# Kernel optimization log

Measured on AMD Instinct MI355X. Metric: run time of the kernel, lower is better.

Reference implementation:

```python
import jax, jax.numpy as jnp
import numpy as np

D_MODEL = 1024
N_HEADS = 16
HEAD_DIM = D_MODEL // N_HEADS
BATCH = 4
SEQ = 2048


def setup_inputs() -> dict:
    key = jax.random.key(0)
    ks = jax.random.split(key, 5)
    # Xavier uniform bound for square d_model x d_model weights
    bound = np.sqrt(6.0 / (D_MODEL + D_MODEL))
    x = jax.random.normal(ks[0], (BATCH, SEQ, D_MODEL), dtype=jnp.float32)
    attention_mask = jnp.ones((BATCH, SEQ), dtype=jnp.int32)
    wq = jax.random.uniform(ks[1], (D_MODEL, D_MODEL), jnp.float32, -bound, bound)
    wk = jax.random.uniform(ks[2], (D_MODEL, D_MODEL), jnp.float32, -bound, bound)
    wv = jax.random.uniform(ks[3], (D_MODEL, D_MODEL), jnp.float32, -bound, bound)
    wo = jax.random.uniform(ks[4], (D_MODEL, D_MODEL), jnp.float32, -bound, bound)
    return {"x": x, "attention_mask": attention_mask,
            "wq": wq, "wk": wk, "wv": wv, "wo": wo}


def reference(x, attention_mask, wq, wk, wv, wo):
    # x: (B, S, D). Linear weights stored torch-style (out, in): y = x @ W^T
    B, S, D = x.shape
    H, Hd = N_HEADS, HEAD_DIM
    scale = np.sqrt(Hd).astype(np.float32)

    def split_heads(t):  # (B,S,D) -> (B,H,S,Hd)
        return t.reshape(B, S, H, Hd).transpose(0, 2, 1, 3)

    q = split_heads(jnp.einsum('bsd,ed->bse', x, wq))
    k = split_heads(jnp.einsum('bsd,ed->bse', x, wk))
    v = split_heads(jnp.einsum('bsd,ed->bse', x, wv))

    scores = jnp.einsum('bhqd,bhkd->bhqk', q, k) / scale  # (B,H,S,S)

    causal = jnp.tril(jnp.ones((S, S), dtype=bool))  # True = keep
    keep = causal[None, None, :, :] & (attention_mask[:, None, None, :] != 0)
    scores = jnp.where(keep, scores, -jnp.inf)

    attn = jax.nn.softmax(scores, axis=-1)  # dropout: eval mode (identity)
    out = jnp.einsum('bhqk,bhkd->bhqd', attn, v)  # (B,H,S,Hd)
    out = out.transpose(0, 2, 1, 3).reshape(B, S, D)
    return jnp.einsum('bsd,ed->bse', out, wo)
```

## Files before the change

kernel.cpp:

```cpp
#include <hip/hip_runtime.h>
#include <cstdint>
#include <cstddef>

#define D_MODEL 1024
#define N_HEADS 16
#define HEAD_DIM 64
#define BATCH 4
#define SEQ 2048
#define M_TOTAL (BATCH * SEQ)

typedef __attribute__((ext_vector_type(8))) short bf16x8;
typedef __attribute__((ext_vector_type(4))) float f32x4;
typedef __attribute__((ext_vector_type(16))) float f32x16;

#define Q_SCALE 0.18033688011112042f

__device__ __forceinline__ unsigned short f2bu(float f) {
    union { float f; unsigned u; } x; x.f = f;
    unsigned r = x.u + 0x7FFFu + ((x.u >> 16) & 1u);
    return (unsigned short)(r >> 16);
}

__device__ __forceinline__ void async16(void* lds, const void* g) {
    __builtin_amdgcn_global_load_lds(
        (const __attribute__((address_space(1))) void*)g,
        (__attribute__((address_space(3))) void*)lds, 16, 0, 0);
}

__global__ __launch_bounds__(256) void cast_all(const float* __restrict__ x,
                                                const float* __restrict__ wq,
                                                const float* __restrict__ wk,
                                                const float* __restrict__ wv,
                                                const float* __restrict__ wo,
                                                unsigned short* __restrict__ dst) {
    const size_t NE = (size_t)M_TOTAL * D_MODEL;
    const size_t WE = (size_t)D_MODEL * D_MODEL;
    size_t i4 = (size_t)blockIdx.x * 256 + threadIdx.x;
    size_t e = i4 * 4;
    const float* src; size_t off;
    if (e < NE) { src = x; off = e; }
    else {
        size_t t = e - NE;
        int r = (int)(t / WE); off = t - (size_t)r * WE;
        src = (r == 0) ? wq : (r == 1) ? wk : (r == 2) ? wv : wo;
    }
    float4 v = *(const float4*)(src + off);
    ushort4 o;
    o.x = f2bu(v.x); o.y = f2bu(v.y); o.z = f2bu(v.z); o.w = f2bu(v.w);
    ((ushort4*)dst)[i4] = o;
}

__global__ __launch_bounds__(256) void qkv_gemm(const unsigned short* __restrict__ X,
                                                const unsigned short* __restrict__ W0,
                                                const unsigned short* __restrict__ W1,
                                                const unsigned short* __restrict__ W2,
                                                unsigned short* __restrict__ Y0,
                                                unsigned short* __restrict__ Y1,
                                                unsigned short* __restrict__ Vt) {
    __shared__ short As[128 * 32];
    __shared__ short Bs[128 * 32];

    const int id = (int)blockIdx.x + 24 * (int)blockIdx.y;
    const int xcd = id & 7, slot = id >> 3;
    const int ty = xcd * 8 + slot / 24;
    const int tx = slot % 24;

    const int sel = tx >> 3;
    const unsigned short* W = (sel == 0) ? W0 : (sel == 1) ? W1 : W2;
    const float scl = (sel == 0) ? Q_SCALE : 1.0f;

    const int tid = threadIdx.x;
    const int w = tid >> 6, lane = tid & 63, quad = lane >> 4, l15 = lane & 15;
    const int wm = w & 1, wn = w >> 1;
    const int rowBase = ty * 128;
    const int colBase = (tx & 7) * 128;

    f32x4 acc[4][4];
#pragma unroll
    for (int mi = 0; mi < 4; ++mi)
#pragma unroll
        for (int ni = 0; ni < 4; ++ni)
#pragma unroll
            for (int e = 0; e < 4; ++e) acc[mi][ni][e] = 0.f;

    for (int k0 = 0; k0 < 1024; k0 += 32) {
        __syncthreads();
#pragma unroll
        for (int l = 0; l < 2; ++l) {
            int c = tid + l * 256;
            int row = c >> 2, ccs = c & 3;
            int cc = ccs ^ ((row >> 1) & 3);
            async16((char*)As + c * 16, X + (size_t)(rowBase + row) * 1024 + k0 + cc * 8);
            async16((char*)Bs + c * 16, W + (size_t)(colBase + row) * 1024 + k0 + cc * 8);
        }
        __syncthreads();

        bf16x8 a[4], b[4];
#pragma unroll
        for (int mi = 0; mi < 4; ++mi) {
            int r = wm * 64 + mi * 16 + l15;
            int slt = quad ^ ((r >> 1) & 3);
            a[mi] = *(const bf16x8*)&As[r * 32 + slt * 8];
        }
#pragma unroll
        for (int ni = 0; ni < 4; ++ni) {
            int r = wn * 64 + ni * 16 + l15;
            int slt = quad ^ ((r >> 1) & 3);
            b[ni] = *(const bf16x8*)&Bs[r * 32 + slt * 8];
        }
#pragma unroll
        for (int mi = 0; mi < 4; ++mi)
#pragma unroll
            for (int ni = 0; ni < 4; ++ni)
                acc[mi][ni] = __builtin_amdgcn_mfma_f32_16x16x32_bf16(a[mi], b[ni], acc[mi][ni], 0, 0, 0);
    }

    if (sel != 2) {
        unsigned short* Y = (sel == 0) ? Y0 : Y1;
#pragma unroll
        for (int mi = 0; mi < 4; ++mi)
#pragma unroll
            for (int ni = 0; ni < 4; ++ni)
#pragma unroll
                for (int reg = 0; reg < 4; ++reg) {
                    int row = rowBase + wm * 64 + mi * 16 + quad * 4 + reg;
                    int col = colBase + wn * 64 + ni * 16 + l15;
                    Y[(size_t)row * 1024 + col] = f2bu(acc[mi][ni][reg] * scl);
                }
    } else {
#pragma unroll
        for (int mi = 0; mi < 4; ++mi) {
            int row0 = rowBase + wm * 64 + mi * 16 + quad * 4;
            int bb = row0 >> 11;
            int s0 = row0 & 2047;
#pragma unroll
            for (int ni = 0; ni < 4; ++ni) {
                int col = colBase + wn * 64 + ni * 16 + l15;
                int hh = col >> 6, dd = col & 63;
                ushort4 pk;
                pk.x = f2bu(acc[mi][ni][0]); pk.y = f2bu(acc[mi][ni][1]);
                pk.z = f2bu(acc[mi][ni][2]); pk.w = f2bu(acc[mi][ni][3]);
                *(ushort4*)(Vt + (((size_t)bb * 16 + hh) * 64 + dd) * SEQ + s0) = pk;
            }
        }
    }
}

__global__ __launch_bounds__(256) void out_gemm(const unsigned short* __restrict__ X,
                                                const unsigned short* __restrict__ W,
                                                float* __restrict__ Y) {
    __shared__ short As[128 * 32];
    __shared__ short Bs[128 * 32];

    const int id = (int)blockIdx.x + 8 * (int)blockIdx.y;
    const int xcd = id & 7, slot = id >> 3;
    const int ty = xcd * 8 + (slot >> 3);
    const int tx = slot & 7;

    const int tid = threadIdx.x;
    const int w = tid >> 6, lane = tid & 63, quad = lane >> 4, l15 = lane & 15;
    const int wm = w & 1, wn = w >> 1;
    const int rowBase = ty * 128;
    const int colBase = tx * 128;

    f32x4 acc[4][4];
#pragma unroll
    for (int mi = 0; mi < 4; ++mi)
#pragma unroll
        for (int ni = 0; ni < 4; ++ni)
#pragma unroll
            for (int e = 0; e < 4; ++e) acc[mi][ni][e] = 0.f;

    for (int k0 = 0; k0 < 1024; k0 += 32) {
        __syncthreads();
#pragma unroll
        for (int l = 0; l < 2; ++l) {
            int c = tid + l * 256;
            int row = c >> 2, ccs = c & 3;
            int cc = ccs ^ ((row >> 1) & 3);
            async16((char*)As + c * 16, X + (size_t)(rowBase + row) * 1024 + k0 + cc * 8);
            async16((char*)Bs + c * 16, W + (size_t)(colBase + row) * 1024 + k0 + cc * 8);
        }
        __syncthreads();

        bf16x8 a[4], b[4];
#pragma unroll
        for (int mi = 0; mi < 4; ++mi) {
            int r = wm * 64 + mi * 16 + l15;
            int slt = quad ^ ((r >> 1) & 3);
            a[mi] = *(const bf16x8*)&As[r * 32 + slt * 8];
        }
#pragma unroll
        for (int ni = 0; ni < 4; ++ni) {
            int r = wn * 64 + ni * 16 + l15;
            int slt = quad ^ ((r >> 1) & 3);
            b[ni] = *(const bf16x8*)&Bs[r * 32 + slt * 8];
        }
#pragma unroll
        for (int mi = 0; mi < 4; ++mi)
#pragma unroll
            for (int ni = 0; ni < 4; ++ni)
                acc[mi][ni] = __builtin_amdgcn_mfma_f32_16x16x32_bf16(a[mi], b[ni], acc[mi][ni], 0, 0, 0);
    }

#pragma unroll
    for (int mi = 0; mi < 4; ++mi)
#pragma unroll
        for (int ni = 0; ni < 4; ++ni)
#pragma unroll
            for (int reg = 0; reg < 4; ++reg) {
                int row = rowBase + wm * 64 + mi * 16 + quad * 4 + reg;
                int col = colBase + wn * 64 + ni * 16 + l15;
                Y[(size_t)row * 1024 + col] = acc[mi][ni][reg];
            }
}

__global__ __launch_bounds__(256) void flash32(const unsigned short* __restrict__ Q,
                                               const unsigned short* __restrict__ K,
                                               const unsigned short* __restrict__ Vt,
                                               const int* __restrict__ mask,
                                               unsigned short* __restrict__ CTX) {
    __shared__ short lds[16384];
    __shared__ float biasS[2][64];
    __shared__ int allokS[2];
    __shared__ int okW[4];

    const int bh = blockIdx.x;
    const int pid = blockIdx.y;
    const int b = bh >> 4;
    const int tid = threadIdx.x;
    const int w = tid >> 6, lane = tid & 63, l31 = lane & 31, lane5 = lane >> 5;

    const size_t qkBase = (size_t)b * SEQ * D_MODEL + (size_t)(bh & 15) * HEAD_DIM;
    const size_t vtBase = (size_t)bh * HEAD_DIM * SEQ;

    {
        int ok = 1;
        for (int i = tid; i < SEQ; i += 256) ok &= (mask[b * SEQ + i] != 0);
        unsigned long long bal = __ballot(ok != 0);
        if (lane == 0) okW[w] = (bal == ~0ull) ? 1 : 0;
    }
    __syncthreads();
    const int allSeq = okW[0] & okW[1] & okW[2] & okW[3];

    int stp[2], stcc[2], stj[2];
#pragma unroll
    for (int l = 0; l < 2; ++l) {
        int c = tid + l * 256;
        int p = c >> 3, sl = c & 7;
        stp[l] = p;
        stcc[l] = sl ^ (p & 7);
        stj[l] = (p & 0x33) | ((p & 4) << 1) | ((p & 8) >> 1);
    }

    for (int phase = 0; phase < 2; ++phase) {
        const int qt = phase ? pid : 15 - pid;
        const int q0 = qt * 128;
        const int iq = q0 + w * 32 + l31;

        bf16x8 qf[4];
#pragma unroll
        for (int ks = 0; ks < 4; ++ks)
            qf[ks] = *(const bf16x8*)(Q + qkBase + (size_t)iq * D_MODEL + ks * 16 + lane5 * 8);

        float mv = -INFINITY, lv = 0.f;
        f32x16 Ot[2];
#pragma unroll
        for (int dt = 0; dt < 2; ++dt)
#pragma unroll
            for (int e = 0; e < 16; ++e) Ot[dt][e] = 0.f;

        const int ktmax = 2 * qt + 1;

        uint4 kreg[2], vreg[2];
        int mreg = 1;
#pragma unroll
        for (int l = 0; l < 2; ++l) {
            kreg[l] = *(const uint4*)(K + qkBase + (size_t)stj[l] * D_MODEL + stcc[l] * 8);
            vreg[l] = *(const uint4*)(Vt + vtBase + (size_t)stp[l] * SEQ + stcc[l] * 8);
        }
        if (!allSeq && tid < 64) mreg = mask[b * SEQ + tid];

        for (int kt = 0; kt <= ktmax; ++kt) {
            const int k0 = kt * 64;
            const int buf = kt & 1;
#pragma unroll
            for (int l = 0; l < 2; ++l) {
                int c = tid + l * 256;
                *(uint4*)((char*)lds + buf * 8192 + c * 16) = kreg[l];
                *(uint4*)((char*)lds + 16384 + buf * 8192 + c * 16) = vreg[l];
            }
            if (!allSeq && tid < 64) {
                biasS[buf][tid] = mreg ? 0.f : -INFINITY;
                unsigned long long bal = __ballot(mreg != 0);
                if (tid == 0) allokS[buf] = (bal == ~0ull) ? 1 : 0;
            }
            if (kt < ktmax) {
                const int kn = k0 + 64;
#pragma unroll
                for (int l = 0; l < 2; ++l) {
                    kreg[l] = *(const uint4*)(K + qkBase + (size_t)(kn + stj[l]) * D_MODEL + stcc[l] * 8);
                    vreg[l] = *(const uint4*)(Vt + vtBase + (size_t)stp[l] * SEQ + kn + stcc[l] * 8);
                }
                if (!allSeq && tid < 64) mreg = mask[b * SEQ + kn + tid];
            }
            __syncthreads();

            if (64 * kt > q0 + 32 * w + 31) continue;

            const short* Ks = lds + buf * 4096;
            const short* Vs = lds + 8192 + buf * 4096;

            const int kHi = q0 + 32 * w + 31 - k0;
            const int nT = (kHi >= 32) ? 2 : 1;
            const int nt = ((kHi >> 4) >= 3 ? 3 : (kHi >> 4)) + 1;

            f32x16 St[2];
            __builtin_amdgcn_s_setprio(1);
#pragma unroll
            for (int T = 0; T < 2; ++T) {
                if (T < nT) {
#pragma unroll
                    for (int e = 0; e < 16; ++e) St[T][e] = 0.f;
#pragma unroll
                    for (int ks = 0; ks < 4; ++ks) {
                        int p = T * 32 + l31;
                        int slot = (ks * 2 + lane5) ^ (p & 7);
                        bf16x8 a = *(const bf16x8*)&Ks[p * 64 + slot * 8];
                        St[T] = __builtin_amdgcn_mfma_f32_32x32x16_bf16(a, qf[ks], St[T], 0, 0, 0);
                    }
                }
            }
            __builtin_amdgcn_s_setprio(0);

            const bool partial = (k0 + 63 > q0 + 32 * w);
            if (partial) {
#pragma unroll
                for (int T = 0; T < 2; ++T)
                    if (T < nT)
#pragma unroll
                        for (int r = 0; r < 16; ++r) {
                            int j = k0 + 32 * T + 16 * (r >> 3) + 8 * lane5 + (r & 7);
                            if (j > iq) St[T][r] = -INFINITY;
                        }
            }
            if (!allSeq && !allokS[buf]) {
#pragma unroll
                for (int T = 0; T < 2; ++T)
                    if (T < nT)
#pragma unroll
                        for (int r = 0; r < 16; ++r)
                            St[T][r] += biasS[buf][32 * T + 16 * (r >> 3) + 8 * lane5 + (r & 7)];
            }

            float tm[2];
#pragma unroll
            for (int T = 0; T < 2; ++T) {
                if (T < nT) {
                    float a0 = fmaxf(fmaxf(St[T][0], St[T][1]), fmaxf(St[T][2], St[T][3]));
                    float a1 = fmaxf(fmaxf(St[T][4], St[T][5]), fmaxf(St[T][6], St[T][7]));
                    float a2 = fmaxf(fmaxf(St[T][8], St[T][9]), fmaxf(St[T][10], St[T][11]));
                    float a3 = fmaxf(fmaxf(St[T][12], St[T][13]), fmaxf(St[T][14], St[T][15]));
                    tm[T] = fmaxf(fmaxf(a0, a1), fmaxf(a2, a3));
                } else tm[T] = -INFINITY;
            }
            float rm = fmaxf(tm[0], tm[1]);
            rm = fmaxf(rm, __shfl_xor(rm, 32));
            float mn = fmaxf(mv, rm);
            if (mn > mv + 8.f) {
                float al = exp2f(mv - mn);
                lv *= al;
#pragma unroll
                for (int dt = 0; dt < 2; ++dt)
#pragma unroll
                    for (int e = 0; e < 16; ++e) Ot[dt][e] *= al;
                mv = mn;
            }
            float rsp[2] = {0.f, 0.f};
#pragma unroll
            for (int T = 0; T < 2; ++T) {
                if (T < nT) {
#pragma unroll
                    for (int r = 0; r < 16; ++r) {
                        float pv = exp2f(St[T][r] - mv);
                        St[T][r] = pv;
                        rsp[T] += pv;
                    }
                }
            }
            float rs = rsp[0] + rsp[1];
            rs += __shfl_xor(rs, 32);
            lv += rs;

            bf16x8 pf[4];
#pragma unroll
            for (int t = 0; t < 4; ++t) {
                if (t < nt) {
                    const int T = t >> 1, hb = t & 1;
                    unsigned u0, u1, u2, u3;
                    asm("v_cvt_pk_bf16_f32 %0, %1, %2" : "=v"(u0)
                        : "v"(St[T][hb * 8 + 0]), "v"(St[T][hb * 8 + 1]));
                    asm("v_cvt_pk_bf16_f32 %0, %1, %2" : "=v"(u1)
                        : "v"(St[T][hb * 8 + 2]), "v"(St[T][hb * 8 + 3]));
                    asm("v_cvt_pk_bf16_f32 %0, %1, %2" : "=v"(u2)
                        : "v"(St[T][hb * 8 + 4]), "v"(St[T][hb * 8 + 5]));
                    asm("v_cvt_pk_bf16_f32 %0, %1, %2" : "=v"(u3)
                        : "v"(St[T][hb * 8 + 6]), "v"(St[T][hb * 8 + 7]));
                    union { unsigned u[4]; bf16x8 v; } pk;
                    pk.u[0] = u0; pk.u[1] = u1; pk.u[2] = u2; pk.u[3] = u3;
                    pf[t] = pk.v;
                }
            }

            __builtin_amdgcn_s_setprio(1);
#pragma unroll
            for (int dt = 0; dt < 2; ++dt)
#pragma unroll
                for (int t = 0; t < 4; ++t) {
                    if (t < nt) {
                        int p = dt * 32 + l31;
                        int slot = (t * 2 + lane5) ^ (p & 7);
                        bf16x8 a = *(const bf16x8*)&Vs[p * 64 + slot * 8];
                        Ot[dt] = __builtin_amdgcn_mfma_f32_32x32x16_bf16(a, pf[t], Ot[dt], 0, 0, 0);
                    }
                }
            __builtin_amdgcn_s_setprio(0);
        }

        __syncthreads();
        const float inv = 1.f / lv;
#pragma unroll
        for (int dt = 0; dt < 2; ++dt)
#pragma unroll
            for (int k = 0; k < 8; ++k) {
                int r0 = 2 * k;
                int d = (r0 & 3) + 4 * lane5 + 8 * (r0 >> 2) + 32 * dt;
                unsigned lo = f2bu(Ot[dt][r0] * inv);
                unsigned hi = f2bu(Ot[dt][r0 + 1] * inv);
                *(unsigned*)&lds[(w * 32 + l31) * 72 + d] = lo | (hi << 16);
            }
        __syncthreads();
#pragma unroll
        for (int k = 0; k < 4; ++k) {
            int id = tid + k * 256;
            int r = id >> 3, cc = id & 7;
            uint4 v = *(const uint4*)&lds[r * 72 + cc * 8];
            *(uint4*)(CTX + qkBase + (size_t)(q0 + r) * D_MODEL + cc * 8) = v;
        }
        __syncthreads();
    }
}

extern "C" void kernel_launch(void* const* d_in, const int* in_sizes, int n_in,
                              void* d_out, int out_size, void* d_ws, size_t ws_size,
                              hipStream_t stream) {
    const float* x  = (const float*)d_in[0];
    const int* mask = (const int*)d_in[1];
    const float* wq = (const float*)d_in[2];
    const float* wk = (const float*)d_in[3];
    const float* wv = (const float*)d_in[4];
    const float* wo = (const float*)d_in[5];
    float* out = (float*)d_out;

    const size_t NE = (size_t)M_TOTAL * D_MODEL;
    const size_t WE = (size_t)D_MODEL * D_MODEL;
    unsigned short* ws  = (unsigned short*)d_ws;
    unsigned short* xb  = ws;
    unsigned short* wqb = xb + NE;
    unsigned short* wkb = wqb + WE;
    unsigned short* wvb = wkb + WE;
    unsigned short* wob = wvb + WE;
    unsigned short* Qb  = wob + WE;
    unsigned short* Kb  = Qb + NE;
    unsigned short* Vtb = Kb + NE;
    unsigned short* CTX = Vtb + NE;

    cast_all<<<(int)((NE + 4 * WE) / 4 / 256), 256, 0, stream>>>(x, wq, wk, wv, wo, ws);

    qkv_gemm<<<dim3(24, M_TOTAL / 128), 256, 0, stream>>>(xb, wqb, wkb, wvb, Qb, Kb, Vtb);

    flash32<<<dim3(64, 8), 256, 0, stream>>>(Qb, Kb, Vtb, mask, CTX);

    out_gemm<<<dim3(D_MODEL / 128, M_TOTAL / 128), 256, 0, stream>>>(CTX, wob, out);
}
```

Baseline: 306.7 us.

## Split flash attention KV range in two halves and merge with a combine kernel

The causal KV range of each query tile is split into two halves, doubling the attention grid so more blocks are resident per CU; the launch bound also requests higher occupancy. Each half writes unnormalized bf16 partial outputs plus per-row max and sum into scratch, reusing the x and wq cast buffers that are dead after the QKV GEMM. A new elementwise kernel rescales and merges the two partials into the context buffer. The merge adds an extra read/write pass over the context plus a launch, and storing unnormalized partials in bf16 adds a rounding step.

```diff
diff --git a/kernel.cpp b/kernel.cpp
--- a/kernel.cpp
+++ b/kernel.cpp
@@ -19,6 +19,9 @@
     union { float f; unsigned u; } x; x.f = f;
     unsigned r = x.u + 0x7FFFu + ((x.u >> 16) & 1u);
     return (unsigned short)(r >> 16);
+}
+__device__ __forceinline__ float bu2f(unsigned hi16bits) {
+    union { unsigned u; float f; } x; x.u = hi16bits; return x.f;
 }
 
 __device__ __forceinline__ void async16(void* lds, const void* g) {
@@ -215,18 +218,21 @@
             }
 }
 
-__global__ __launch_bounds__(256) void flash32(const unsigned short* __restrict__ Q,
-                                               const unsigned short* __restrict__ K,
-                                               const unsigned short* __restrict__ Vt,
-                                               const int* __restrict__ mask,
-                                               unsigned short* __restrict__ CTX) {
+__global__ __launch_bounds__(256, 4) void flash32(const unsigned short* __restrict__ Q,
+                                                  const unsigned short* __restrict__ K,
+                                                  const unsigned short* __restrict__ Vt,
+                                                  const int* __restrict__ mask,
+                                                  unsigned short* __restrict__ P0,
+                                                  unsigned short* __restrict__ P1,
+                                                  float2* __restrict__ ml) {
     __shared__ short lds[16384];
     __shared__ float biasS[2][64];
     __shared__ int allokS[2];
     __shared__ int okW[4];
 
     const int bh = blockIdx.x;
-    const int pid = blockIdx.y;
+    const int pid = (int)blockIdx.y & 7;
+    const int kvHalf = (int)blockIdx.y >> 3;
     const int b = bh >> 4;
     const int tid = threadIdx.x;
     const int w = tid >> 6, lane = tid & 63, l31 = lane & 31, lane5 = lane >> 5;
@@ -258,6 +264,9 @@
         const int q0 = qt * 128;
         const int iq = q0 + w * 32 + l31;
 
+        const int klo = kvHalf * (qt + 1);
+        const int kend = klo + qt;
+
         bf16x8 qf[4];
 #pragma unroll
         for (int ks = 0; ks < 4; ++ks)
@@ -270,18 +279,16 @@
 #pragma unroll
             for (int e = 0; e < 16; ++e) Ot[dt][e] = 0.f;
 
-        const int ktmax = 2 * qt + 1;
-
         uint4 kreg[2], vreg[2];
         int mreg = 1;
 #pragma unroll
         for (int l = 0; l < 2; ++l) {
-            kreg[l] = *(const uint4*)(K + qkBase + (size_t)stj[l] * D_MODEL + stcc[l] * 8);
-            vreg[l] = *(const uint4*)(Vt + vtBase + (size_t)stp[l] * SEQ + stcc[l] * 8);
-        }
-        if (!allSeq && tid < 64) mreg = mask[b * SEQ + tid];
-
-        for (int kt = 0; kt <= ktmax; ++kt) {
+            kreg[l] = *(const uint4*)(K + qkBase + (size_t)(klo * 64 + stj[l]) * D_MODEL + stcc[l] * 8);
+            vreg[l] = *(const uint4*)(Vt + vtBase + (size_t)stp[l] * SEQ + klo * 64 + stcc[l] * 8);
+        }
+        if (!allSeq && tid < 64) mreg = mask[b * SEQ + klo * 64 + tid];
+
+        for (int kt = klo; kt <= kend; ++kt) {
             const int k0 = kt * 64;
             const int buf = kt & 1;
 #pragma unroll
@@ -295,7 +302,7 @@
                 unsigned long long bal = __ballot(mreg != 0);
                 if (tid == 0) allokS[buf] = (bal == ~0ull) ? 1 : 0;
             }
-            if (kt < ktmax) {
+            if (kt < kend) {
                 const int kn = k0 + 64;
 #pragma unroll
                 for (int l = 0; l < 2; ++l) {
@@ -428,27 +435,65 @@
         }
 
         __syncthreads();
-        const float inv = 1.f / lv;
+        unsigned short* dst = kvHalf ? P1 : P0;
 #pragma unroll
         for (int dt = 0; dt < 2; ++dt)
 #pragma unroll
             for (int k = 0; k < 8; ++k) {
                 int r0 = 2 * k;
                 int d = (r0 & 3) + 4 * lane5 + 8 * (r0 >> 2) + 32 * dt;
-                unsigned lo = f2bu(Ot[dt][r0] * inv);
-                unsigned hi = f2bu(Ot[dt][r0 + 1] * inv);
+                unsigned lo = f2bu(Ot[dt][r0]);
+                unsigned hi = f2bu(Ot[dt][r0 + 1]);
                 *(unsigned*)&lds[(w * 32 + l31) * 72 + d] = lo | (hi << 16);
             }
+        if (lane < 32) {
+            float2 v; v.x = mv; v.y = lv;
+            ml[(((size_t)(kvHalf * 4 + b)) * 16 + (bh & 15)) * 2048 + (q0 + w * 32 + l31)] = v;
+        }
         __syncthreads();
 #pragma unroll
         for (int k = 0; k < 4; ++k) {
             int id = tid + k * 256;
             int r = id >> 3, cc = id & 7;
             uint4 v = *(const uint4*)&lds[r * 72 + cc * 8];
-            *(uint4*)(CTX + qkBase + (size_t)(q0 + r) * D_MODEL + cc * 8) = v;
-        }
-        __syncthreads();
-    }
+            *(uint4*)(dst + qkBase + (size_t)(q0 + r) * D_MODEL + cc * 8) = v;
+        }
+        __syncthreads();
+    }
+}
+
+__global__ __launch_bounds__(256) void flash_combine(unsigned short* __restrict__ CTX,
+                                                     const unsigned short* __restrict__ P1,
+                                                     const float2* __restrict__ ml) {
+    size_t i8 = (size_t)blockIdx.x * 256 + threadIdx.x;
+    size_t e = i8 * 8;
+    int row = (int)(e >> 10);
+    int col = (int)(e & 1023);
+    int head = col >> 6;
+    int b = row >> 11, s = row & 2047;
+
+    float2 a0 = ml[(((size_t)b) * 16 + head) * 2048 + s];
+    float2 a1 = ml[(((size_t)(4 + b)) * 16 + head) * 2048 + s];
+    float m = fmaxf(a0.x, a1.x);
+    float f0 = exp2f(a0.x - m);
+    float f1 = exp2f(a1.x - m);
+    float l = a0.y * f0 + a1.y * f1;
+    float inv = 1.f / l;
+    f0 *= inv; f1 *= inv;
+
+    uint4 u0 = *(const uint4*)(CTX + e);
+    uint4 u1 = *(const uint4*)(P1 + e);
+    unsigned o[4];
+    unsigned uu0[4] = {u0.x, u0.y, u0.z, u0.w};
+    unsigned uu1[4] = {u1.x, u1.y, u1.z, u1.w};
+#pragma unroll
+    for (int j = 0; j < 4; ++j) {
+        float xl = bu2f(uu0[j] << 16) * f0 + bu2f(uu1[j] << 16) * f1;
+        float xh = bu2f(uu0[j] & 0xFFFF0000u) * f0 + bu2f(uu1[j] & 0xFFFF0000u) * f1;
+        o[j] = f2bu(xl) | ((unsigned)f2bu(xh) << 16);
+    }
+    uint4 ov; ov.x = o[0]; ov.y = o[1]; ov.z = o[2]; ov.w = o[3];
+    *(uint4*)(CTX + e) = ov;
 }
 
 extern "C" void kernel_launch(void* const* d_in, const int* in_sizes, int n_in,
@@ -479,7 +524,9 @@
 
     qkv_gemm<<<dim3(24, M_TOTAL / 128), 256, 0, stream>>>(xb, wqb, wkb, wvb, Qb, Kb, Vtb);
 
-    flash32<<<dim3(64, 8), 256, 0, stream>>>(Qb, Kb, Vtb, mask, CTX);
+    flash32<<<dim3(64, 16), 256, 0, stream>>>(Qb, Kb, Vtb, mask, CTX, xb, (float2*)wqb);
+
+    flash_combine<<<(int)(NE / 8 / 256), 256, 0, stream>>>(CTX, xb, (const float2*)wqb);
 
     out_gemm<<<dim3(D_MODEL / 128, M_TOTAL / 128), 256, 0, stream>>>(CTX, wob, out);
 }
```

Result: slower. 394.1 us (+28.5%).

## Rewrite QKV projection as 256x256-tile, 512-thread, 4-stage pipelined GEMM

Applied to the files above, without the earlier changes.

Replaces the 128x128 single-buffered QKV GEMM with a 256x256 tile kernel using 8 waves and a 4-slot LDS ring, prefetched three k-steps ahead via async global-to-LDS loads. Each k-step is split into interleaved half-stages, with explicit vmcnt waits, barriers and setprio around the MFMA blocks. This targets the load-wait stalls and the low data reuse of the old kernel. It uses all 128 KB of LDS and more accumulator registers, which lowers occupancy, and the launch shrinks to 384 blocks.

```diff
diff --git a/kernel.cpp b/kernel.cpp
--- a/kernel.cpp
+++ b/kernel.cpp
@@ -50,87 +50,180 @@
     ((ushort4*)dst)[i4] = o;
 }
 
-__global__ __launch_bounds__(256) void qkv_gemm(const unsigned short* __restrict__ X,
-                                                const unsigned short* __restrict__ W0,
-                                                const unsigned short* __restrict__ W1,
-                                                const unsigned short* __restrict__ W2,
-                                                unsigned short* __restrict__ Y0,
-                                                unsigned short* __restrict__ Y1,
-                                                unsigned short* __restrict__ Vt) {
-    __shared__ short As[128 * 32];
-    __shared__ short Bs[128 * 32];
-
-    const int id = (int)blockIdx.x + 24 * (int)blockIdx.y;
+__device__ __forceinline__ void stageHalfA(const unsigned short* __restrict__ src,
+                                           int srcRowBase, int j, int tid,
+                                           const int* gp, const int* gcc, short* lds) {
+    if (j >= 32) return;
+#pragma unroll
+    for (int l = 0; l < 2; ++l)
+        async16((char*)lds + ((j & 3) << 14) + (tid + l * 512) * 16,
+                src + (size_t)(srcRowBase + gp[l]) * 1024 + j * 32 + gcc[l] * 8);
+}
+__device__ __forceinline__ void stageHalfB(const unsigned short* __restrict__ src,
+                                           int srcRowBase, int j, int tid,
+                                           const int* gp, const int* gcc, short* lds) {
+    if (j >= 32) return;
+#pragma unroll
+    for (int l = 0; l < 2; ++l)
+        async16((char*)lds + 65536 + ((j & 3) << 14) + (tid + l * 512) * 16,
+                src + (size_t)(srcRowBase + gp[l]) * 1024 + j * 32 + gcc[l] * 8);
+}
+
+__global__ __launch_bounds__(512) void qkv256(const unsigned short* __restrict__ X,
+                                              const unsigned short* __restrict__ W0,
+                                              const unsigned short* __restrict__ W1,
+                                              const unsigned short* __restrict__ W2,
+                                              unsigned short* __restrict__ Y0,
+                                              unsigned short* __restrict__ Y1,
+                                              unsigned short* __restrict__ Vt) {
+    __shared__ short lds[65536];
+
+    const int id = (int)blockIdx.x;
     const int xcd = id & 7, slot = id >> 3;
-    const int ty = xcd * 8 + slot / 24;
-    const int tx = slot % 24;
-
-    const int sel = tx >> 3;
+    const int ty = xcd * 4 + slot / 12;
+    const int r12 = slot % 12;
+    const int sel = r12 >> 2;
+    const int tx = r12 & 3;
     const unsigned short* W = (sel == 0) ? W0 : (sel == 1) ? W1 : W2;
     const float scl = (sel == 0) ? Q_SCALE : 1.0f;
+    const int rowBase = ty * 256;
+    const int colBase = tx * 256;
 
     const int tid = threadIdx.x;
-    const int w = tid >> 6, lane = tid & 63, quad = lane >> 4, l15 = lane & 15;
-    const int wm = w & 1, wn = w >> 1;
-    const int rowBase = ty * 128;
-    const int colBase = (tx & 7) * 128;
-
-    f32x4 acc[4][4];
-#pragma unroll
-    for (int mi = 0; mi < 4; ++mi)
+    const int wid = tid >> 6, lane = tid & 63, quad = lane >> 4, l15 = lane & 15;
+    const int wm = wid >> 2, wn = wid & 3;
+
+    int gp[2], gcc[2];
+#pragma unroll
+    for (int l = 0; l < 2; ++l) {
+        int g = tid + l * 512;
+        gp[l] = g >> 2;
+        gcc[l] = (g & 3) ^ ((gp[l] >> 1) & 3);
+    }
+
+    f32x4 acc[8][4];
+#pragma unroll
+    for (int mi = 0; mi < 8; ++mi)
 #pragma unroll
         for (int ni = 0; ni < 4; ++ni)
 #pragma unroll
             for (int e = 0; e < 4; ++e) acc[mi][ni][e] = 0.f;
 
-    for (int k0 = 0; k0 < 1024; k0 += 32) {
-        __syncthreads();
-#pragma unroll
-        for (int l = 0; l < 2; ++l) {
-            int c = tid + l * 256;
-            int row = c >> 2, ccs = c & 3;
-            int cc = ccs ^ ((row >> 1) & 3);
-            async16((char*)As + c * 16, X + (size_t)(rowBase + row) * 1024 + k0 + cc * 8);
-            async16((char*)Bs + c * 16, W + (size_t)(colBase + row) * 1024 + k0 + cc * 8);
-        }
-        __syncthreads();
-
-        bf16x8 a[4], b[4];
-#pragma unroll
-        for (int mi = 0; mi < 4; ++mi) {
-            int r = wm * 64 + mi * 16 + l15;
-            int slt = quad ^ ((r >> 1) & 3);
-            a[mi] = *(const bf16x8*)&As[r * 32 + slt * 8];
-        }
+    stageHalfA(X, rowBase, 0, tid, gp, gcc, lds);
+    stageHalfB(W, colBase, 0, tid, gp, gcc, lds);
+    stageHalfA(X, rowBase, 1, tid, gp, gcc, lds);
+    stageHalfB(W, colBase, 1, tid, gp, gcc, lds);
+    stageHalfA(X, rowBase, 2, tid, gp, gcc, lds);
+    stageHalfB(W, colBase, 2, tid, gp, gcc, lds);
+    asm volatile("s_waitcnt vmcnt(8)" ::: "memory");
+    __builtin_amdgcn_s_barrier();
+
+    for (int kt = 0; kt < 16; ++kt) {
+        const int qA = (2 * kt) & 3;
+        const int qB = (2 * kt + 1) & 3;
+        bf16x8 afr[4], bfr[4];
+
+        stageHalfA(X, rowBase, 2 * kt + 3, tid, gp, gcc, lds);
 #pragma unroll
         for (int ni = 0; ni < 4; ++ni) {
-            int r = wn * 64 + ni * 16 + l15;
-            int slt = quad ^ ((r >> 1) & 3);
-            b[ni] = *(const bf16x8*)&Bs[r * 32 + slt * 8];
-        }
-#pragma unroll
-        for (int mi = 0; mi < 4; ++mi)
+            int rb = wn * 64 + ni * 16 + l15;
+            int sl = quad ^ ((rb >> 1) & 3);
+            bfr[ni] = *(const bf16x8*)&lds[32768 + qA * 8192 + rb * 32 + sl * 8];
+        }
+#pragma unroll
+        for (int i = 0; i < 4; ++i) {
+            int r = wm * 128 + i * 16 + l15;
+            int sl = quad ^ ((r >> 1) & 3);
+            afr[i] = *(const bf16x8*)&lds[qA * 8192 + r * 32 + sl * 8];
+        }
+        __builtin_amdgcn_s_barrier();
+        __builtin_amdgcn_s_setprio(1);
+#pragma unroll
+        for (int i = 0; i < 4; ++i)
 #pragma unroll
             for (int ni = 0; ni < 4; ++ni)
-                acc[mi][ni] = __builtin_amdgcn_mfma_f32_16x16x32_bf16(a[mi], b[ni], acc[mi][ni], 0, 0, 0);
+                acc[i][ni] = __builtin_amdgcn_mfma_f32_16x16x32_bf16(afr[i], bfr[ni], acc[i][ni], 0, 0, 0);
+        __builtin_amdgcn_s_setprio(0);
+        __builtin_amdgcn_s_barrier();
+
+        stageHalfB(W, colBase, 2 * kt + 3, tid, gp, gcc, lds);
+#pragma unroll
+        for (int i = 0; i < 4; ++i) {
+            int r = wm * 128 + (4 + i) * 16 + l15;
+            int sl = quad ^ ((r >> 1) & 3);
+            afr[i] = *(const bf16x8*)&lds[qA * 8192 + r * 32 + sl * 8];
+        }
+        __builtin_amdgcn_s_barrier();
+        __builtin_amdgcn_s_setprio(1);
+#pragma unroll
+        for (int i = 0; i < 4; ++i)
+#pragma unroll
+            for (int ni = 0; ni < 4; ++ni)
+                acc[4 + i][ni] = __builtin_amdgcn_mfma_f32_16x16x32_bf16(afr[i], bfr[ni], acc[4 + i][ni], 0, 0, 0);
+        __builtin_amdgcn_s_setprio(0);
+        if (kt < 15) { asm volatile("s_waitcnt vmcnt(8)" ::: "memory"); }
+        else         { asm volatile("s_waitcnt vmcnt(0)" ::: "memory"); }
+        __builtin_amdgcn_s_barrier();
+
+        stageHalfA(X, rowBase, 2 * kt + 4, tid, gp, gcc, lds);
+#pragma unroll
+        for (int ni = 0; ni < 4; ++ni) {
+            int rb = wn * 64 + ni * 16 + l15;
+            int sl = quad ^ ((rb >> 1) & 3);
+            bfr[ni] = *(const bf16x8*)&lds[32768 + qB * 8192 + rb * 32 + sl * 8];
+        }
+#pragma unroll
+        for (int i = 0; i < 4; ++i) {
+            int r = wm * 128 + i * 16 + l15;
+            int sl = quad ^ ((r >> 1) & 3);
+            afr[i] = *(const bf16x8*)&lds[qB * 8192 + r * 32 + sl * 8];
+        }
+        __builtin_amdgcn_s_barrier();
+        __builtin_amdgcn_s_setprio(1);
+#pragma unroll
+        for (int i = 0; i < 4; ++i)
+#pragma unroll
+            for (int ni = 0; ni < 4; ++ni)
+                acc[i][ni] = __builtin_amdgcn_mfma_f32_16x16x32_bf16(afr[i], bfr[ni], acc[i][ni], 0, 0, 0);
+        __builtin_amdgcn_s_setprio(0);
+        __builtin_amdgcn_s_barrier();
+
+        stageHalfB(W, colBase, 2 * kt + 4, tid, gp, gcc, lds);
+#pragma unroll
+        for (int i = 0; i < 4; ++i) {
+            int r = wm * 128 + (4 + i) * 16 + l15;
+            int sl = quad ^ ((r >> 1) & 3);
+            afr[i] = *(const bf16x8*)&lds[qB * 8192 + r * 32 + sl * 8];
+        }
+        __builtin_amdgcn_s_barrier();
+        __builtin_amdgcn_s_setprio(1);
+#pragma unroll
+        for (int i = 0; i < 4; ++i)
+#pragma unroll
+            for (int ni = 0; ni < 4; ++ni)
+                acc[4 + i][ni] = __builtin_amdgcn_mfma_f32_16x16x32_bf16(afr[i], bfr[ni], acc[4 + i][ni], 0, 0, 0);
+        __builtin_amdgcn_s_setprio(0);
+        if (kt < 14)      { asm volatile("s_waitcnt vmcnt(8)" ::: "memory"); }
+        else if (kt == 14){ asm volatile("s_waitcnt vmcnt(4)" ::: "memory"); }
+        __builtin_amdgcn_s_barrier();
     }
 
     if (sel != 2) {
         unsigned short* Y = (sel == 0) ? Y0 : Y1;
 #pragma unroll
-        for (int mi = 0; mi < 4; ++mi)
+        for (int mi = 0; mi < 8; ++mi)
 #pragma unroll
             for (int ni = 0; ni < 4; ++ni)
 #pragma unroll
                 for (int reg = 0; reg < 4; ++reg) {
-                    int row = rowBase + wm * 64 + mi * 16 + quad * 4 + reg;
+                    int row = rowBase + wm * 128 + mi * 16 + quad * 4 + reg;
                     int col = colBase + wn * 64 + ni * 16 + l15;
                     Y[(size_t)row * 1024 + col] = f2bu(acc[mi][ni][reg] * scl);
                 }
     } else {
 #pragma unroll
-        for (int mi = 0; mi < 4; ++mi) {
-            int row0 = rowBase + wm * 64 + mi * 16 + quad * 4;
+        for (int mi = 0; mi < 8; ++mi) {
+            int row0 = rowBase + wm * 128 + mi * 16 + quad * 4;
             int bb = row0 >> 11;
             int s0 = row0 & 2047;
 #pragma unroll
@@ -477,7 +570,7 @@
 
     cast_all<<<(int)((NE + 4 * WE) / 4 / 256), 256, 0, stream>>>(x, wq, wk, wv, wo, ws);
 
-    qkv_gemm<<<dim3(24, M_TOTAL / 128), 256, 0, stream>>>(xb, wqb, wkb, wvb, Qb, Kb, Vtb);
+    qkv256<<<dim3(384), 512, 0, stream>>>(xb, wqb, wkb, wvb, Qb, Kb, Vtb);
 
     flash32<<<dim3(64, 8), 256, 0, stream>>>(Qb, Kb, Vtb, mask, CTX);
 
```

Result: no change. 307.8 us (+0.4%).

## Double-buffer LDS tiles in QKV and output projection GEMMs

Applied to the files above, without the earlier changes.

Both projection GEMMs now use two LDS buffers per operand. The global-to-LDS async load for the next K tile is issued before the MFMA work on the current tile, so each iteration has one barrier instead of two and load latency can overlap compute. Per-thread staging offsets are precomputed outside the loop. The cost is double the LDS footprint per block, which may reduce occupancy, and correctness depends on the barrier also waiting for the outstanding async loads.

```diff
diff --git a/kernel.cpp b/kernel.cpp
--- a/kernel.cpp
+++ b/kernel.cpp
@@ -57,8 +57,8 @@
                                                 unsigned short* __restrict__ Y0,
                                                 unsigned short* __restrict__ Y1,
                                                 unsigned short* __restrict__ Vt) {
-    __shared__ short As[128 * 32];
-    __shared__ short Bs[128 * 32];
+    __shared__ short As[2][128 * 32];
+    __shared__ short Bs[2][128 * 32];
 
     const int id = (int)blockIdx.x + 24 * (int)blockIdx.y;
     const int xcd = id & 7, slot = id >> 3;
@@ -75,6 +75,14 @@
     const int rowBase = ty * 128;
     const int colBase = (tx & 7) * 128;
 
+    int stRow[2], stCc[2];
+#pragma unroll
+    for (int l = 0; l < 2; ++l) {
+        int c = tid + l * 256;
+        stRow[l] = c >> 2;
+        stCc[l] = (c & 3) ^ ((stRow[l] >> 1) & 3);
+    }
+
     f32x4 acc[4][4];
 #pragma unroll
     for (int mi = 0; mi < 4; ++mi)
@@ -83,36 +91,48 @@
 #pragma unroll
             for (int e = 0; e < 4; ++e) acc[mi][ni][e] = 0.f;
 
-    for (int k0 = 0; k0 < 1024; k0 += 32) {
-        __syncthreads();
-#pragma unroll
-        for (int l = 0; l < 2; ++l) {
-            int c = tid + l * 256;
-            int row = c >> 2, ccs = c & 3;
-            int cc = ccs ^ ((row >> 1) & 3);
-            async16((char*)As + c * 16, X + (size_t)(rowBase + row) * 1024 + k0 + cc * 8);
-            async16((char*)Bs + c * 16, W + (size_t)(colBase + row) * 1024 + k0 + cc * 8);
-        }
-        __syncthreads();
+#pragma unroll
+    for (int l = 0; l < 2; ++l) {
+        int c = tid + l * 256;
+        async16((char*)As[0] + c * 16, X + (size_t)(rowBase + stRow[l]) * 1024 + stCc[l] * 8);
+        async16((char*)Bs[0] + c * 16, W + (size_t)(colBase + stRow[l]) * 1024 + stCc[l] * 8);
+    }
+    __syncthreads();
+
+    for (int kt = 0; kt < 32; ++kt) {
+        const int buf = kt & 1;
+        if (kt < 31) {
+            const int kn = (kt + 1) * 32;
+#pragma unroll
+            for (int l = 0; l < 2; ++l) {
+                int c = tid + l * 256;
+                async16((char*)As[buf ^ 1] + c * 16,
+                        X + (size_t)(rowBase + stRow[l]) * 1024 + kn + stCc[l] * 8);
+                async16((char*)Bs[buf ^ 1] + c * 16,
+                        W + (size_t)(colBase + stRow[l]) * 1024 + kn + stCc[l] * 8);
+            }
+        }
 
         bf16x8 a[4], b[4];
 #pragma unroll
         for (int mi = 0; mi < 4; ++mi) {
             int r = wm * 64 + mi * 16 + l15;
             int slt = quad ^ ((r >> 1) & 3);
-            a[mi] = *(const bf16x8*)&As[r * 32 + slt * 8];
+            a[mi] = *(const bf16x8*)&As[buf][r * 32 + slt * 8];
         }
 #pragma unroll
         for (int ni = 0; ni < 4; ++ni) {
             int r = wn * 64 + ni * 16 + l15;
             int slt = quad ^ ((r >> 1) & 3);
-            b[ni] = *(const bf16x8*)&Bs[r * 32 + slt * 8];
+            b[ni] = *(const bf16x8*)&Bs[buf][r * 32 + slt * 8];
         }
 #pragma unroll
         for (int mi = 0; mi < 4; ++mi)
 #pragma unroll
             for (int ni = 0; ni < 4; ++ni)
                 acc[mi][ni] = __builtin_amdgcn_mfma_f32_16x16x32_bf16(a[mi], b[ni], acc[mi][ni], 0, 0, 0);
+
+        __syncthreads();
     }
 
     if (sel != 2) {
@@ -149,8 +169,8 @@
 __global__ __launch_bounds__(256) void out_gemm(const unsigned short* __restrict__ X,
                                                 const unsigned short* __restrict__ W,
                                                 float* __restrict__ Y) {
-    __shared__ short As[128 * 32];
-    __shared__ short Bs[128 * 32];
+    __shared__ short As[2][128 * 32];
+    __shared__ short Bs[2][128 * 32];
 
     const int id = (int)blockIdx.x + 8 * (int)blockIdx.y;
     const int xcd = id & 7, slot = id >> 3;
@@ -163,6 +183,14 @@
     const int rowBase = ty * 128;
     const int colBase = tx * 128;
 
+    int stRow[2], stCc[2];
+#pragma unroll
+    for (int l = 0; l < 2; ++l) {
+        int c = tid + l * 256;
+        stRow[l] = c >> 2;
+        stCc[l] = (c & 3) ^ ((stRow[l] >> 1) & 3);
+    }
+
     f32x4 acc[4][4];
 #pragma unroll
     for (int mi = 0; mi < 4; ++mi)
@@ -171,36 +199,48 @@
 #pragma unroll
             for (int e = 0; e < 4; ++e) acc[mi][ni][e] = 0.f;
 
-    for (int k0 = 0; k0 < 1024; k0 += 32) {
-        __syncthreads();
-#pragma unroll
-        for (int l = 0; l < 2; ++l) {
-            int c = tid + l * 256;
-            int row = c >> 2, ccs = c & 3;
-            int cc = ccs ^ ((row >> 1) & 3);
-            async16((char*)As + c * 16, X + (size_t)(rowBase + row) * 1024 + k0 + cc * 8);
-            async16((char*)Bs + c * 16, W + (size_t)(colBase + row) * 1024 + k0 + cc * 8);
-        }
-        __syncthreads();
+#pragma unroll
+    for (int l = 0; l < 2; ++l) {
+        int c = tid + l * 256;
+        async16((char*)As[0] + c * 16, X + (size_t)(rowBase + stRow[l]) * 1024 + stCc[l] * 8);
+        async16((char*)Bs[0] + c * 16, W + (size_t)(colBase + stRow[l]) * 1024 + stCc[l] * 8);
+    }
+    __syncthreads();
+
+    for (int kt = 0; kt < 32; ++kt) {
+        const int buf = kt & 1;
+        if (kt < 31) {
+            const int kn = (kt + 1) * 32;
+#pragma unroll
+            for (int l = 0; l < 2; ++l) {
+                int c = tid + l * 256;
+                async16((char*)As[buf ^ 1] + c * 16,
+                        X + (size_t)(rowBase + stRow[l]) * 1024 + kn + stCc[l] * 8);
+                async16((char*)Bs[buf ^ 1] + c * 16,
+                        W + (size_t)(colBase + stRow[l]) * 1024 + kn + stCc[l] * 8);
+            }
+        }
 
         bf16x8 a[4], b[4];
 #pragma unroll
         for (int mi = 0; mi < 4; ++mi) {
             int r = wm * 64 + mi * 16 + l15;
             int slt = quad ^ ((r >> 1) & 3);
-            a[mi] = *(const bf16x8*)&As[r * 32 + slt * 8];
+            a[mi] = *(const bf16x8*)&As[buf][r * 32 + slt * 8];
         }
 #pragma unroll
         for (int ni = 0; ni < 4; ++ni) {
             int r = wn * 64 + ni * 16 + l15;
             int slt = quad ^ ((r >> 1) & 3);
-            b[ni] = *(const bf16x8*)&Bs[r * 32 + slt * 8];
+            b[ni] = *(const bf16x8*)&Bs[buf][r * 32 + slt * 8];
         }
 #pragma unroll
         for (int mi = 0; mi < 4; ++mi)
 #pragma unroll
             for (int ni = 0; ni < 4; ++ni)
                 acc[mi][ni] = __builtin_amdgcn_mfma_f32_16x16x32_bf16(a[mi], b[ni], acc[mi][ni], 0, 0, 0);
+
+        __syncthreads();
     }
 
 #pragma unroll
```

New measurement: 307.3 us (median of 2 runs). About the same (+0.2%).
